# Kernel tuning notes

Measured on AMD Instinct MI355X. Metric: run time of the kernel, lower is better.

Reference implementation:

```python
import jax, jax.numpy as jnp
import numpy as np

DIM = 1024
GROUPS = 32
EPS = 1e-5


def setup_inputs() -> dict:
    key = jax.random.key(0)
    ks = jax.random.split(key, 12)
    b, c, h, w = 16, DIM, 32, 32  # h*w must equal DIM for GroupNorm(32, dim) on (b, hw, c)
    x = jax.random.normal(ks[0], (b, c, h, w), dtype=jnp.float32)
    # GroupNorm affine params: num_channels = dim (applied along hw axis, which == dim)
    gamma = jnp.ones((DIM,), dtype=jnp.float32)
    beta = jnp.zeros((DIM,), dtype=jnp.float32)
    init = lambda k: jax.random.normal(k, (DIM, DIM), dtype=jnp.float32) * 0.02
    Wq, Wk, Wv, Wo = init(ks[1]), init(ks[2]), init(ks[3]), init(ks[4])
    bq = jax.random.normal(ks[5], (DIM,), dtype=jnp.float32) * 0.02
    bk = jax.random.normal(ks[6], (DIM,), dtype=jnp.float32) * 0.02
    bv = jax.random.normal(ks[7], (DIM,), dtype=jnp.float32) * 0.02
    bo = jax.random.normal(ks[8], (DIM,), dtype=jnp.float32) * 0.02
    return {"x": x, "gamma": gamma, "beta": beta,
            "Wq": Wq, "bq": bq, "Wk": Wk, "bk": bk,
            "Wv": Wv, "bv": bv, "Wo": Wo, "bo": bo}


def _group_norm(x, gamma, beta):
    # x: (b, N, c) where N == num_channels (torch GroupNorm normalizes groups along dim 1)
    b, N, c = x.shape
    xg = x.reshape(b, GROUPS, (N // GROUPS) * c)
    mean = xg.mean(-1, keepdims=True)
    var = xg.var(-1, keepdims=True)
    xn = ((xg - mean) * jax.lax.rsqrt(var + EPS)).reshape(b, N, c)
    return xn * gamma[None, :, None] + beta[None, :, None]


def reference(x, gamma, beta, Wq, bq, Wk, bk, Wv, bv, Wo, bo):
    b, c, h, w = x.shape
    xs = x.reshape(b, c, h * w).transpose(0, 2, 1)  # (b, N, c), N = h*w
    norm_x = _group_norm(xs, gamma, beta)
    q = norm_x @ Wq.T + bq
    k = norm_x @ Wk.T + bk
    v = norm_x @ Wv.T + bv
    attn = jnp.einsum('bqd,bkd->bqk', q, k) * (c ** -0.5)
    attn = jax.nn.softmax(attn, axis=-1)
    # Faithful to original: 'bqk,bvd->bqd' sums k and v independently (no contraction between them)
    out = jnp.einsum('bqk,bvd->bqd', attn, v)
    out = out @ Wo.T + bo  # Dropout(p=0.0) is identity
    return out.transpose(0, 2, 1).reshape(b, c, h, w)
```

## Files before the change

### kernel.cpp

```cpp
#include <hip/hip_runtime.h>


#define BATCH 16
#define CH    1024
#define NHW   1024
#define G     32
#define NPG   32
#define EPG   (NPG*CH)
#define EPSV  1e-5f

__global__ __launch_bounds__(1024, 8) void k1_stats_colsum(
    const float* __restrict__ x, const float* __restrict__ gamma,
    const float* __restrict__ beta, float* __restrict__ colsum)
{
    const int blk  = blockIdx.x;
    const int t    = threadIdx.x;
    const int lane = t & 63, wave = t >> 6;
    const int b    = blk >> 5, g = blk & 31;
    const int n4   = t & 7;
    const int c0   = t >> 3;

    __shared__ float pch[CH];
    __shared__ float r1[16], r2[16], rb[16];

    const float4* xg = reinterpret_cast<const float4*>(x + (size_t)b * (CH * NHW) + g * NPG);
    const float4  gm = reinterpret_cast<const float4*>(gamma + g * NPG)[n4];

    float4 vb[8];
    #pragma unroll
    for (int k = 0; k < 8; k++)
        vb[k] = xg[(c0 + k * 128) * (NHW / 4) + n4];

    float s1 = 0.f, s2 = 0.f;
    #pragma unroll
    for (int k = 0; k < 8; k++) {
        const float4 v = vb[k];
        const int ch = c0 + k * 128;
        s1 += v.x + v.y + v.z + v.w;
        s2 += v.x * v.x + v.y * v.y + v.z * v.z + v.w * v.w;
        float p = v.x * gm.x + v.y * gm.y + v.z * gm.z + v.w * gm.w;
        p += __shfl_xor(p, 1);
        p += __shfl_xor(p, 2);
        p += __shfl_xor(p, 4);
        if (n4 == 0) pch[ch] = p;
    }
    float bsum = beta[t];
    #pragma unroll
    for (int m = 1; m < 64; m <<= 1) {
        s1 += __shfl_xor(s1, m); s2 += __shfl_xor(s2, m); bsum += __shfl_xor(bsum, m);
    }
    if (lane == 0) { r1[wave] = s1; r2[wave] = s2; rb[wave] = bsum; }
    __syncthreads();

    float S1 = 0.f, S2 = 0.f, SB = 0.f;
    #pragma unroll
    for (int w = 0; w < 16; w++) { S1 += r1[w]; S2 += r2[w]; SB += rb[w]; }
    const float mean = S1 * (1.f / EPG);
    const float var  = S2 * (1.f / EPG) - mean * mean;
    const float inv  = rsqrtf(var + EPSV);
    float sg = gm.x + gm.y + gm.z + gm.w;
    sg += __shfl_xor(sg, 1);
    sg += __shfl_xor(sg, 2);
    sg += __shfl_xor(sg, 4);
    const float cshare = SB * (1.f / 32.f) - inv * mean * sg;

    atomicAdd(&colsum[b * CH + t], inv * pch[t] + cshare);
}

__global__ __launch_bounds__(256) void k2_matvec_v(
    const float* __restrict__ Wv, const float* __restrict__ bv,
    const float* __restrict__ colsum, float* __restrict__ S)
{
    const int t = threadIdx.x;
    const int wave = t >> 6, lane = t & 63;
    const int d = blockIdx.x * 4 + wave;
    const float4* wrow = reinterpret_cast<const float4*>(Wv + (size_t)d * CH);
    const float4* cs4  = reinterpret_cast<const float4*>(colsum);
    float acc[BATCH];
    #pragma unroll
    for (int b = 0; b < BATCH; b++) acc[b] = 0.f;
    #pragma unroll
    for (int i = 0; i < 4; i++) {
        int e4 = i * 64 + lane;
        float4 w = wrow[e4];
        #pragma unroll
        for (int b = 0; b < BATCH; b++) {
            float4 c = cs4[b * 256 + e4];
            acc[b] += w.x * c.x + w.y * c.y + w.z * c.z + w.w * c.w;
        }
    }
    #pragma unroll
    for (int b = 0; b < BATCH; b++) {
        float a = acc[b];
        #pragma unroll
        for (int m = 1; m < 64; m <<= 1) a += __shfl_xor(a, m);
        if (lane == 0) S[b * CH + d] = a + (float)NHW * bv[d];
    }
}

__global__ __launch_bounds__(1024, 8) void k3_out(
    const float* __restrict__ Wo, const float* __restrict__ bo,
    const float* __restrict__ S, float* __restrict__ out)
{
    const int blk  = blockIdx.x;
    const int t    = threadIdx.x;
    const int lane = t & 63, wave = t >> 6;
    const int b    = blk >> 5, slab = blk & 31;

    __shared__ float smem[CH];
    if (t < 256)
        reinterpret_cast<float4*>(smem)[t] =
            reinterpret_cast<const float4*>(S + (size_t)b * CH)[t];
    __syncthreads();

    const int d0 = slab * 32 + wave * 2;
    const float4* s4 = reinterpret_cast<const float4*>(smem);
    #pragma unroll
    for (int j = 0; j < 2; j++) {
        const int d = d0 + j;
        const float4* wrow = reinterpret_cast<const float4*>(Wo + (size_t)d * CH);
        float a = 0.f;
        #pragma unroll
        for (int i = 0; i < 4; i++) {
            int e4 = i * 64 + lane;
            float4 w = wrow[e4];
            float4 c = s4[e4];
            a += w.x * c.x + w.y * c.y + w.z * c.z + w.w * c.w;
        }
        #pragma unroll
        for (int m = 1; m < 64; m <<= 1) a += __shfl_xor(a, m);
        const float val = a + bo[d];
        float4 v4 = make_float4(val, val, val, val);
        float4* op = reinterpret_cast<float4*>(out + ((size_t)b * CH + d) * NHW);
        #pragma unroll
        for (int i = 0; i < 4; i++) op[i * 64 + lane] = v4;
    }
}

extern "C" void kernel_launch(void* const* d_in, const int* in_sizes, int n_in,
                              void* d_out, int out_size, void* d_ws, size_t ws_size,
                              hipStream_t stream)
{
    const float* x     = (const float*)d_in[0];
    const float* gamma = (const float*)d_in[1];
    const float* beta  = (const float*)d_in[2];
    const float* Wv    = (const float*)d_in[7];
    const float* bv    = (const float*)d_in[8];
    const float* Wo    = (const float*)d_in[9];
    const float* bo    = (const float*)d_in[10];
    float* out = (float*)d_out;

    char* ws = (char*)d_ws;
    float* colsum = (float*)ws;
    float* Sbuf   = (float*)(ws + 65536);

    hipMemsetAsync(colsum, 0, BATCH * CH * sizeof(float), stream);
    k1_stats_colsum<<<BATCH * G, 1024, 0, stream>>>(x, gamma, beta, colsum);
    k2_matvec_v    <<<256,       256, 0, stream>>>(Wv, bv, colsum, Sbuf);
    k3_out         <<<BATCH * G, 1024, 0, stream>>>(Wo, bo, Sbuf, out);
}
```

Measured before the change: 159.4 us.

## Replace atomics and memset with per-group partials reduced in matvec kernel; nontemporal output stores

The stats kernel now writes a per-(batch, group) partial column-sum buffer instead of atomically accumulating into a zeroed buffer, so the memset launch and the atomics go away. The V matvec kernel first reduces the 32 group partials for its batch into shared memory, then each block computes 128 output rows for that batch. This re-reads Wv once per batch from cache. The output broadcast stores switch to nontemporal stores to reduce cache pollution on the 64MB write.

```diff
diff --git a/kernel.cpp b/kernel.cpp
--- a/kernel.cpp
+++ b/kernel.cpp
@@ -9,9 +9,11 @@
 #define EPG   (NPG*CH)
 #define EPSV  1e-5f
 
-__global__ __launch_bounds__(1024, 8) void k1_stats_colsum(
+typedef float floatx4 __attribute__((ext_vector_type(4)));
+
+__global__ __launch_bounds__(1024, 8) void k1_partials(
     const float* __restrict__ x, const float* __restrict__ gamma,
-    const float* __restrict__ beta, float* __restrict__ colsum)
+    const float* __restrict__ beta, float* __restrict__ pbg)
 {
     const int blk  = blockIdx.x;
     const int t    = threadIdx.x;
@@ -64,34 +66,39 @@
     sg += __shfl_xor(sg, 4);
     const float cshare = SB * (1.f / 32.f) - inv * mean * sg;
 
-    atomicAdd(&colsum[b * CH + t], inv * pch[t] + cshare);
+    pbg[(size_t)blk * CH + t] = inv * pch[t] + cshare;
 }
 
-__global__ __launch_bounds__(256) void k2_matvec_v(
-    const float* __restrict__ Wv, const float* __restrict__ bv,
-    const float* __restrict__ colsum, float* __restrict__ S)
+__global__ __launch_bounds__(1024, 8) void k2_reduce_matvec(
+    const float* __restrict__ pbg, const float* __restrict__ Wv,
+    const float* __restrict__ bv, float* __restrict__ S)
 {
-    const int t = threadIdx.x;
-    const int wave = t >> 6, lane = t & 63;
-    const int d = blockIdx.x * 4 + wave;
-    const float4* wrow = reinterpret_cast<const float4*>(Wv + (size_t)d * CH);
-    const float4* cs4  = reinterpret_cast<const float4*>(colsum);
-    float acc[BATCH];
+    const int blk = blockIdx.x, t = threadIdx.x;
+    const int lane = t & 63, wave = t >> 6;
+    const int b = blk >> 3, s8 = blk & 7;
+
+    __shared__ float cs[CH];
+    float acc = 0.f;
     #pragma unroll
-    for (int b = 0; b < BATCH; b++) acc[b] = 0.f;
+    for (int g = 0; g < G; ++g)
+        acc += pbg[((size_t)b * G + g) * CH + t];
+    cs[t] = acc;
+    __syncthreads();
+
+    const float4* cs4 = reinterpret_cast<const float4*>(cs);
+    const int d0 = s8 * 128 + wave * 8;
     #pragma unroll
-    for (int i = 0; i < 4; i++) {
-        int e4 = i * 64 + lane;
-        float4 w = wrow[e4];
+    for (int j = 0; j < 8; j++) {
+        const int d = d0 + j;
+        const float4* wrow = reinterpret_cast<const float4*>(Wv + (size_t)d * CH);
+        float a = 0.f;
         #pragma unroll
-        for (int b = 0; b < BATCH; b++) {
-            float4 c = cs4[b * 256 + e4];
-            acc[b] += w.x * c.x + w.y * c.y + w.z * c.z + w.w * c.w;
+        for (int i = 0; i < 4; i++) {
+            int e4 = i * 64 + lane;
+            float4 w = wrow[e4];
+            float4 c = cs4[e4];
+            a += w.x * c.x + w.y * c.y + w.z * c.z + w.w * c.w;
         }
-    }
-    #pragma unroll
-    for (int b = 0; b < BATCH; b++) {
-        float a = acc[b];
         #pragma unroll
         for (int m = 1; m < 64; m <<= 1) a += __shfl_xor(a, m);
         if (lane == 0) S[b * CH + d] = a + (float)NHW * bv[d];
@@ -130,10 +137,11 @@
         #pragma unroll
         for (int m = 1; m < 64; m <<= 1) a += __shfl_xor(a, m);
         const float val = a + bo[d];
-        float4 v4 = make_float4(val, val, val, val);
-        float4* op = reinterpret_cast<float4*>(out + ((size_t)b * CH + d) * NHW);
+        floatx4 v4 = { val, val, val, val };
+        floatx4* op = reinterpret_cast<floatx4*>(out + ((size_t)b * CH + d) * NHW);
         #pragma unroll
-        for (int i = 0; i < 4; i++) op[i * 64 + lane] = v4;
+        for (int i = 0; i < 4; i++)
+            __builtin_nontemporal_store(v4, op + i * 64 + lane);
     }
 }
 
@@ -151,11 +159,10 @@
     float* out = (float*)d_out;
 
     char* ws = (char*)d_ws;
-    float* colsum = (float*)ws;
-    float* Sbuf   = (float*)(ws + 65536);
+    float* pbg  = (float*)ws;
+    float* Sbuf = (float*)(ws + (size_t)2 * 1024 * 1024);
 
-    hipMemsetAsync(colsum, 0, BATCH * CH * sizeof(float), stream);
-    k1_stats_colsum<<<BATCH * G, 1024, 0, stream>>>(x, gamma, beta, colsum);
-    k2_matvec_v    <<<256,       256, 0, stream>>>(Wv, bv, colsum, Sbuf);
-    k3_out         <<<BATCH * G, 1024, 0, stream>>>(Wo, bo, Sbuf, out);
+    k1_partials     <<<BATCH * G, 1024, 0, stream>>>(x, gamma, beta, pbg);
+    k2_reduce_matvec<<<BATCH * 8, 1024, 0, stream>>>(pbg, Wv, bv, Sbuf);
+    k3_out          <<<BATCH * G, 1024, 0, stream>>>(Wo, bo, Sbuf, out);
 }
```

New measurement: 164.7 us. 3.4% more time.
